# Optimization experiments

Hardware: AMD Instinct MI355X
Metric: run time of the kernel (lower is better)

The kernel has to match this reference:

```python
import jax, jax.numpy as jnp
import numpy as np

H = 12          # num_attention_heads
D = 64          # attention_head_size
HID = H * D     # hidden_size = 768
M = 1024        # max_position_embeddings


def setup_inputs() -> dict:
    key = jax.random.key(0)
    ks = jax.random.split(key, 9)
    B, S = 4, 1024
    s = 0.02
    return {
        "hidden_states": jax.random.normal(ks[0], (B, S, HID), jnp.float32),
        "attention_mask": jnp.zeros((B, 1, 1, S), jnp.float32),
        "Wq": jax.random.normal(ks[1], (HID, HID), jnp.float32) * s,
        "bq": jnp.zeros((HID,), jnp.float32),
        "Wk": jax.random.normal(ks[2], (HID, HID), jnp.float32) * s,
        "bk": jnp.zeros((HID,), jnp.float32),
        "Wv": jax.random.normal(ks[3], (HID, HID), jnp.float32) * s,
        "bv": jnp.zeros((HID,), jnp.float32),
        "dist_emb": jax.random.normal(ks[4], (2 * M - 1, D), jnp.float32) * s,
    }


def reference(hidden_states, attention_mask, Wq, bq, Wk, bk, Wv, bv, dist_emb):
    B, S, _ = hidden_states.shape

    def heads(x):  # [B,S,HID] -> [B,H,S,D]
        return x.reshape(B, S, H, D).transpose(0, 2, 1, 3)

    q = heads(hidden_states @ Wq + bq)
    k = heads(hidden_states @ Wk + bk)
    v = heads(hidden_states @ Wv + bv)

    # raw dot-product scores [B,H,S,S]
    scores = jnp.einsum('bhld,bhrd->bhlr', q, k)

    # relative_key_query positional bias
    pos = jnp.arange(S)
    distance = pos[:, None] - pos[None, :] + (M - 1)   # [S,S] in [0, 2M-2]
    pe = dist_emb[distance]                            # [S,S,D]
    scores = scores + jnp.einsum('bhld,lrd->bhlr', q, pe) \
                    + jnp.einsum('bhrd,lrd->bhlr', k, pe)

    scores = scores / jnp.sqrt(jnp.asarray(D, scores.dtype)) + attention_mask
    probs = jax.nn.softmax(scores, axis=-1)            # dropout is identity in eval

    ctx = jnp.einsum('bhlr,bhrd->bhld', probs, v)      # [B,H,S,D]
    ctx = ctx.transpose(0, 2, 1, 3).reshape(B, S, HID)
    return ctx, probs
```

## Files before the change

### kernel.cpp

```cpp
#include <hip/hip_runtime.h>
#include <hip/hip_bf16.h>

#define DEVFN __device__ __forceinline__

typedef __bf16 bf16x8 __attribute__((ext_vector_type(8)));
typedef float f32x4 __attribute__((ext_vector_type(4)));
typedef unsigned short ushort8 __attribute__((ext_vector_type(8)));
typedef unsigned short us4 __attribute__((ext_vector_type(4)));

namespace {

constexpr int S = 1024;
constexpr int HID = 768;
constexpr int NH = 12;
constexpr int HD = 64;
constexpr float SC = 0.4246609f;
constexpr float LOG2E = 1.44269504f;

DEVFN unsigned short f2bf(float f) {
  union { float f; unsigned u; } v; v.f = f;
  unsigned r = v.u + 0x7FFF + ((v.u >> 16) & 1);
  return (unsigned short)(r >> 16);
}

DEVFN float bf2f(unsigned short u) {
  union { unsigned u; float f; } v; v.u = ((unsigned)u) << 16; return v.f;
}

DEVFN f32x4 zero4() { return f32x4{0.f, 0.f, 0.f, 0.f}; }

DEVFN f32x4 mfma_bf16(bf16x8 a, bf16x8 b, f32x4 c) {
  return __builtin_amdgcn_mfma_f32_16x16x32_bf16(a, b, c, 0, 0, 0);
}

DEVFN void gload16(void* lds_base, const void* gsrc) {
  __builtin_amdgcn_global_load_lds(
      (const __attribute__((address_space(1))) void*)gsrc,
      (__attribute__((address_space(3))) void*)lds_base, 16, 0, 0);
}

DEVFN bf16x8 frag_ld(const char* tile, int row, int ch) {
  int chs = ch ^ (row & 7);
  return *(const bf16x8*)(tile + row * 128 + chs * 16);
}

__global__ void k0_cvt_x(const float* __restrict__ x, unsigned short* __restrict__ xb) {
  size_t i = (size_t)(blockIdx.x * 256 + threadIdx.x) * 8;
  float4 a = *(const float4*)(x + i);
  float4 c = *(const float4*)(x + i + 4);
  ushort8 o;
  o[0] = f2bf(a.x); o[1] = f2bf(a.y); o[2] = f2bf(a.z); o[3] = f2bf(a.w);
  o[4] = f2bf(c.x); o[5] = f2bf(c.y); o[6] = f2bf(c.z); o[7] = f2bf(c.w);
  *(ushort8*)(xb + i) = o;
}

__global__ void k0_cvt_pe(const float* __restrict__ de, unsigned short* __restrict__ peb) {
  size_t i = (size_t)(blockIdx.x * 256 + threadIdx.x) * 8;
  int row = (int)(i >> 6);
  ushort8 o;
  if (row < 2047) {
    float4 a = *(const float4*)(de + i);
    float4 c = *(const float4*)(de + i + 4);
    o[0] = f2bf(a.x * SC); o[1] = f2bf(a.y * SC); o[2] = f2bf(a.z * SC); o[3] = f2bf(a.w * SC);
    o[4] = f2bf(c.x * SC); o[5] = f2bf(c.y * SC); o[6] = f2bf(c.z * SC); o[7] = f2bf(c.w * SC);
  } else {
    o = ushort8{0, 0, 0, 0, 0, 0, 0, 0};
  }
  *(ushort8*)(peb + i) = o;
}

__global__ __launch_bounds__(256) void k0_wt(const float* __restrict__ Wq,
                                             const float* __restrict__ Wk,
                                             const float* __restrict__ Wv,
                                             unsigned short* __restrict__ wt) {
  __shared__ float t[64][65];
  int bidx = blockIdx.x;
  int sec = bidx / 144, rem = bidx % 144;
  int ktb = rem / 12, ntb = rem % 12;
  const float* W = (sec == 0) ? Wq : ((sec == 1) ? Wk : Wv);
  int k0 = ktb * 64, n0 = ntb * 64;
  int tid = threadIdx.x;
  #pragma unroll
  for (int p = 0; p < 4; ++p) {
    int id = p * 256 + tid;
    int row = id >> 4, ch = id & 15;
    float4 v = *(const float4*)(W + (size_t)(k0 + row) * 768 + n0 + ch * 4);
    t[row][ch * 4 + 0] = v.x; t[row][ch * 4 + 1] = v.y;
    t[row][ch * 4 + 2] = v.z; t[row][ch * 4 + 3] = v.w;
  }
  __syncthreads();
  #pragma unroll
  for (int p = 0; p < 2; ++p) {
    int id = p * 256 + tid;
    int nrow = id >> 3, c8 = id & 7;
    ushort8 o;
    #pragma unroll
    for (int i = 0; i < 8; ++i) o[i] = f2bf(t[c8 * 8 + i][nrow]);
    *(ushort8*)(wt + (size_t)(sec * 768 + n0 + nrow) * 768 + k0 + c8 * 8) = o;
  }
}

__global__ __launch_bounds__(256) void k1_qkv(
    const unsigned short* __restrict__ xb, const unsigned short* __restrict__ wt,
    const float* __restrict__ bq, const float* __restrict__ bk, const float* __restrict__ bv,
    unsigned short* __restrict__ q_ws, unsigned short* __restrict__ k_ws,
    unsigned short* __restrict__ vt_ws) {
  __shared__ char ldsA[8192], ldsB[8192];
  const int tid = threadIdx.x, lane = tid & 63, wv = tid >> 6;
  const int row16 = lane & 15, cgrp = lane >> 4;
  const int ntb = blockIdx.x % 36, mtb = blockIdx.x / 36;
  const int sec = ntb / 12;
  const int n0 = ntb * 64;
  const int m0 = mtb * 64;

  f32x4 acc[4] = {zero4(), zero4(), zero4(), zero4()};

  for (int k0 = 0; k0 < 768; k0 += 64) {
    #pragma unroll
    for (int c = 0; c < 2; ++c) {
      int cc = (wv * 2 + c) * 64 + lane;
      int row = cc >> 3, ch = cc & 7, chs = ch ^ (row & 7);
      gload16(ldsA + (wv * 2 + c) * 1024, xb + (size_t)(m0 + row) * 768 + k0 + chs * 8);
      gload16(ldsB + (wv * 2 + c) * 1024, wt + (size_t)(n0 + row) * 768 + k0 + chs * 8);
    }
    __syncthreads();
    if (sec < 2) {
      bf16x8 af[2];
      #pragma unroll
      for (int k2 = 0; k2 < 2; ++k2) af[k2] = frag_ld(ldsA, wv * 16 + row16, k2 * 4 + cgrp);
      #pragma unroll
      for (int nt = 0; nt < 4; ++nt)
        #pragma unroll
        for (int k2 = 0; k2 < 2; ++k2) {
          bf16x8 bf = frag_ld(ldsB, nt * 16 + row16, k2 * 4 + cgrp);
          acc[nt] = mfma_bf16(af[k2], bf, acc[nt]);
        }
    } else {
      bf16x8 af[2];
      #pragma unroll
      for (int k2 = 0; k2 < 2; ++k2) af[k2] = frag_ld(ldsB, wv * 16 + row16, k2 * 4 + cgrp);
      #pragma unroll
      for (int mt = 0; mt < 4; ++mt)
        #pragma unroll
        for (int k2 = 0; k2 < 2; ++k2) {
          bf16x8 bx = frag_ld(ldsA, mt * 16 + row16, k2 * 4 + cgrp);
          acc[mt] = mfma_bf16(af[k2], bx, acc[mt]);
        }
    }
    __syncthreads();
  }

  if (sec < 2) {
    unsigned short* dst = (sec == 0) ? q_ws : k_ws;
    const float* bias = (sec == 0) ? bq : bk;
    int nl0 = (ntb % 12) * 64;
    #pragma unroll
    for (int nt = 0; nt < 4; ++nt) {
      int nn = nl0 + nt * 16 + row16;
      float bb = bias[nn];
      int hh = nn >> 6, dd = nn & 63;
      #pragma unroll
      for (int j = 0; j < 4; ++j) {
        int m = m0 + wv * 16 + cgrp * 4 + j;
        int b_ = m >> 10, s_ = m & 1023;
        dst[(size_t)((b_ * 12 + hh) * 1024 + s_) * 64 + dd] = f2bf((acc[nt][j] + bb) * SC);
      }
    }
  } else {
    int nl0 = (ntb % 12) * 64;
    #pragma unroll
    for (int j = 0; j < 4; ++j) {
      int nn = nl0 + wv * 16 + cgrp * 4 + j;
      float bb = bv[nn];
      int hh = nn >> 6, dd = nn & 63;
      #pragma unroll
      for (int mt = 0; mt < 4; ++mt) {
        int m = m0 + mt * 16 + row16;
        int b_ = m >> 10, s_ = m & 1023;
        vt_ws[(size_t)((b_ * 12 + hh) * 64 + dd) * 1024 + s_] = f2bf(acc[mt][j] + bb);
      }
    }
  }
}

__global__ __launch_bounds__(512) void k2_score(
    const unsigned short* __restrict__ q_ws, const unsigned short* __restrict__ k_ws,
    const unsigned short* __restrict__ peb, const float* __restrict__ mask,
    unsigned short* __restrict__ p_out, float* __restrict__ rsum_part) {
  __shared__ __align__(16) char stage_lds[40960];
  __shared__ unsigned short p_sh[2][64 * 64];
  __shared__ float rsum_sh[4][64];

  const int tid = threadIdx.x, lane = tid & 63;
  const int wv8 = tid >> 6;
  const int quad = wv8 >> 2;
  const int wv = wv8 & 3;
  const int wl = wv >> 1, wr = wv & 1;
  const int row16 = lane & 15, cgrp = lane >> 4;

  const int bid = blockIdx.x;
  const int swz = (bid & 7) * 768 + (bid >> 3);
  const int rq = swz & 7, lt = (swz >> 3) & 15, bh = swz >> 7;
  const int b = bh / NH;
  const int l0 = lt * 64;
  const int rt = rq * 2 + quad;
  const int r0 = rt * 64;

  const unsigned short* qh = q_ws + (size_t)bh * S * HD;
  const unsigned short* khp = k_ws + (size_t)bh * S * HD;
  const float* maskb = mask + b * S;

  char* k_lds = stage_lds + quad * 8192;
  char* pe_lds = stage_lds + 16384;
  const int peoff = 64 * (1 - quad);

  #pragma unroll
  for (int c = 0; c < 2; ++c) {
    int cc = (wv * 2 + c) * 64 + lane;
    int row = cc >> 3, ch = cc & 7, chs = ch ^ (row & 7);
    gload16(k_lds + (wv * 2 + c) * 1024, khp + (size_t)(r0 + row) * HD + chs * 8);
  }
  {
    int mU = l0 - rq * 128 - 64 + 960;
    #pragma unroll
    for (int c = 0; c < 3; ++c) {
      int cc = (wv8 * 3 + c) * 64 + lane;
      int row = cc >> 3, ch = cc & 7, chs = ch ^ (row & 7);
      gload16(pe_lds + (wv8 * 3 + c) * 1024, peb + (size_t)(mU + row) * HD + chs * 8);
    }
  }

  bf16x8 qf[2][2];
  #pragma unroll
  for (int ltl = 0; ltl < 2; ++ltl)
    #pragma unroll
    for (int k2 = 0; k2 < 2; ++k2)
      qf[ltl][k2] = *(const bf16x8*)(qh + (size_t)(l0 + wl * 32 + ltl * 16 + row16) * HD +
                                     k2 * 32 + cgrp * 8);
  __syncthreads();

  bf16x8 kf[2][2], pef[4][2];
  #pragma unroll
  for (int rtl = 0; rtl < 2; ++rtl)
    #pragma unroll
    for (int k2 = 0; k2 < 2; ++k2)
      kf[rtl][k2] = frag_ld(k_lds, wr * 32 + rtl * 16 + row16, k2 * 4 + cgrp);
  const int qb = (wl - wr) * 32 + 32 + peoff;
  #pragma unroll
  for (int jt = 0; jt < 4; ++jt)
    #pragma unroll
    for (int k2 = 0; k2 < 2; ++k2)
      pef[jt][k2] = frag_ld(pe_lds, qb + jt * 16 + row16, k2 * 4 + cgrp);
  __syncthreads();

  unsigned short* s3w = (unsigned short*)stage_lds + wv8 * (64 * 36);

  #pragma unroll
  for (int rtl = 0; rtl < 2; ++rtl)
    #pragma unroll
    for (int jt = 0; jt < 4; ++jt) {
      f32x4 a3 = zero4();
      a3 = mfma_bf16(kf[rtl][0], pef[jt][0], a3);
      a3 = mfma_bf16(kf[rtl][1], pef[jt][1], a3);
      us4 o;
      o[0] = f2bf(a3[0]); o[1] = f2bf(a3[1]); o[2] = f2bf(a3[2]); o[3] = f2bf(a3[3]);
      *(us4*)(s3w + (jt * 16 + row16) * 36 + rtl * 16 + cgrp * 4) = o;
    }

  f32x4 s1[2][2];
  #pragma unroll
  for (int ltl = 0; ltl < 2; ++ltl)
    #pragma unroll
    for (int rtl = 0; rtl < 2; ++rtl) {
      f32x4 a1 = zero4();
      a1 = mfma_bf16(qf[ltl][0], kf[rtl][0], a1);
      a1 = mfma_bf16(qf[ltl][1], kf[rtl][1], a1);
      s1[ltl][rtl] = a1;
    }
  f32x4 s2[2][4];
  #pragma unroll
  for (int ltl = 0; ltl < 2; ++ltl)
    #pragma unroll
    for (int jt = 0; jt < 4; ++jt) {
      f32x4 a2 = zero4();
      a2 = mfma_bf16(qf[ltl][0], pef[jt][0], a2);
      a2 = mfma_bf16(qf[ltl][1], pef[jt][1], a2);
      s2[ltl][jt] = a2;
    }

  float rs[2][4] = {};
  #pragma unroll
  for (int rtl = 0; rtl < 2; ++rtl) {
    float mval = maskb[r0 + wr * 32 + rtl * 16 + row16] * LOG2E;
    #pragma unroll
    for (int ltl = 0; ltl < 2; ++ltl) {
      const int jtA = ltl - rtl + 1;
      #pragma unroll
      for (int j = 0; j < 4; ++j) {
        int dl = ltl * 16 + cgrp * 4 + j;
        int dr = rtl * 16 + row16;
        int jjq = dl - dr + 31;
        int src = (lane & 48) | (jjq & 15);
        float vA = __shfl(s2[ltl][jtA][j], src, 64);
        float vB = __shfl(s2[ltl][jtA + 1][j], src, 64);
        float b1 = ((jjq >> 4) == jtA) ? vA : vB;
        float b2 = bf2f(s3w[jjq * 36 + dr]);
        float p = exp2f(s1[ltl][rtl][j] + b1 + b2 + mval);
        rs[ltl][j] += p;
        int dlb = wl * 32 + dl, drb = wr * 32 + dr;
        p_sh[quad][dlb * 64 + (drb ^ ((dlb & 7) << 3))] = f2bf(p);
      }
    }
  }

  #pragma unroll
  for (int ltl = 0; ltl < 2; ++ltl)
    #pragma unroll
    for (int j = 0; j < 4; ++j) {
      float v = rs[ltl][j];
      v += __shfl_xor(v, 1, 64);
      v += __shfl_xor(v, 2, 64);
      v += __shfl_xor(v, 4, 64);
      v += __shfl_xor(v, 8, 64);
      rs[ltl][j] = v;
    }
  if (row16 == 0) {
    #pragma unroll
    for (int ltl = 0; ltl < 2; ++ltl)
      #pragma unroll
      for (int j = 0; j < 4; ++j)
        rsum_sh[quad * 2 + wr][wl * 32 + ltl * 16 + cgrp * 4 + j] = rs[ltl][j];
  }
  __syncthreads();

  if (tid < 64)
    rsum_part[((size_t)(bh * 16 + lt) * 64 + tid) * 8 + rq] =
        rsum_sh[0][tid] + rsum_sh[1][tid] + rsum_sh[2][tid] + rsum_sh[3][tid];

  {
    const int t256 = tid & 255;
    #pragma unroll
    for (int p2 = 0; p2 < 2; ++p2) {
      int id = p2 * 256 + t256, dl = id >> 3, c = id & 7;
      uint4 w = *(const uint4*)((const char*)p_sh[quad] + dl * 128 + (c ^ (dl & 7)) * 16);
      *(uint4*)(p_out + ((size_t)bh * S + l0 + dl) * S + r0 + c * 8) = w;
    }
  }
}

__global__ __launch_bounds__(256) void k3_pv(
    const unsigned short* __restrict__ p_in, const unsigned short* __restrict__ vt_ws,
    const float* __restrict__ rsum_part, float* __restrict__ out_ctx,
    float* __restrict__ out_probs) {
  __shared__ char p_sh[2][8192];
  __shared__ float inv_sh[64];

  const int tid = threadIdx.x, lane = tid & 63, wv = tid >> 6;
  const int row16 = lane & 15, cgrp = lane >> 4;
  const int bid = blockIdx.x;
  const int swz = (bid & 7) * 96 + (bid >> 3);
  const int lt = swz & 15, bh = swz >> 4;
  const int b = bh / NH, h = bh % NH;
  const int l0 = lt * 64;

  const unsigned short* vth = vt_ws + (size_t)bh * HD * S;
  float* probs_bh = out_probs + (size_t)bh * S * S;

  if (tid < 64) {
    const float4* pp =
        (const float4*)(rsum_part + ((size_t)(bh * 16 + lt) * 64 + tid) * 8);
    float4 v0 = pp[0], v1 = pp[1];
    inv_sh[tid] = 1.0f / (v0.x + v0.y + v0.z + v0.w + v1.x + v1.y + v1.z + v1.w);
  }

  auto stage = [&](char* buf, int r0) {
    #pragma unroll
    for (int c = 0; c < 2; ++c) {
      int cc = (wv * 2 + c) * 64 + lane;
      int row = cc >> 3, ch = cc & 7, chs = ch ^ (row & 7);
      gload16(buf + (wv * 2 + c) * 1024,
              p_in + ((size_t)bh * S + l0 + row) * S + r0 + chs * 8);
    }
  };

  stage(p_sh[0], 0);
  __syncthreads();

  f32x4 ctxacc[4] = {zero4(), zero4(), zero4(), zero4()};

  for (int rt = 0; rt < 16; ++rt) {
    const int r0 = rt * 64, cur = rt & 1;
    if (rt < 15) stage(p_sh[cur ^ 1], r0 + 64);
    const char* cb = p_sh[cur];

    #pragma unroll
    for (int p2 = 0; p2 < 2; ++p2) {
      int id = p2 * 256 + tid, dl = id >> 3, c = id & 7;
      uint4 w = *(const uint4*)(cb + dl * 128 + (c ^ (dl & 7)) * 16);
      const unsigned short* pu = (const unsigned short*)&w;
      float iv = inv_sh[dl];
      float* dst = probs_bh + (size_t)(l0 + dl) * S + r0 + c * 8;
      float4 lo{bf2f(pu[0]) * iv, bf2f(pu[1]) * iv, bf2f(pu[2]) * iv, bf2f(pu[3]) * iv};
      float4 hi{bf2f(pu[4]) * iv, bf2f(pu[5]) * iv, bf2f(pu[6]) * iv, bf2f(pu[7]) * iv};
      *(float4*)dst = lo; *(float4*)(dst + 4) = hi;
    }

    {
      int lrow = wv * 16 + row16;
      bf16x8 pa[2];
      #pragma unroll
      for (int kc = 0; kc < 2; ++kc) {
        int ch = kc * 4 + cgrp, chs = ch ^ (lrow & 7);
        pa[kc] = *(const bf16x8*)(cb + lrow * 128 + chs * 16);
      }
      #pragma unroll
      for (int dt = 0; dt < 4; ++dt) {
        bf16x8 vb0 = *(const bf16x8*)(vth + (size_t)(dt * 16 + row16) * S + r0 + cgrp * 8);
        bf16x8 vb1 = *(const bf16x8*)(vth + (size_t)(dt * 16 + row16) * S + r0 + 32 + cgrp * 8);
        ctxacc[dt] = mfma_bf16(pa[0], vb0, ctxacc[dt]);
        ctxacc[dt] = mfma_bf16(pa[1], vb1, ctxacc[dt]);
      }
    }
    __syncthreads();
  }

  #pragma unroll
  for (int dt = 0; dt < 4; ++dt)
    #pragma unroll
    for (int j = 0; j < 4; ++j) {
      int lr = wv * 16 + cgrp * 4 + j;
      out_ctx[((size_t)(b * S + l0 + lr)) * HID + h * HD + dt * 16 + row16] =
          ctxacc[dt][j] * inv_sh[lr];
    }
}

}

extern "C" void kernel_launch(void* const* d_in, const int* in_sizes, int n_in,
                              void* d_out, int out_size, void* d_ws, size_t ws_size,
                              hipStream_t stream) {
  const float* hidden = (const float*)d_in[0];
  const float* mask   = (const float*)d_in[1];
  const float* Wq = (const float*)d_in[2];
  const float* bq = (const float*)d_in[3];
  const float* Wk = (const float*)d_in[4];
  const float* bk = (const float*)d_in[5];
  const float* Wv = (const float*)d_in[6];
  const float* bv = (const float*)d_in[7];
  const float* de = (const float*)d_in[8];

  unsigned short* ws = (unsigned short*)d_ws;
  unsigned short* q_ws  = ws;
  unsigned short* k_ws  = ws + 3145728;
  unsigned short* vt_ws = ws + 6291456;
  unsigned short* xb    = ws + 9437184;
  unsigned short* wt    = ws + 12582912;
  unsigned short* peb   = ws + 14352384;
  float* rsum_part = (float*)(ws + 14483456);
  unsigned short* p_ws  = ws + 16056320;

  float* outc = (float*)d_out;
  float* outp = outc + (size_t)4 * 1024 * 768;

  hipLaunchKernelGGL(k0_cvt_x, dim3(1536), dim3(256), 0, stream, hidden, xb);
  hipLaunchKernelGGL(k0_cvt_pe, dim3(64), dim3(256), 0, stream, de, peb);
  hipLaunchKernelGGL(k0_wt, dim3(432), dim3(256), 0, stream, Wq, Wk, Wv, wt);
  hipLaunchKernelGGL(k1_qkv, dim3(2304), dim3(256), 0, stream,
                     xb, wt, bq, bk, bv, q_ws, k_ws, vt_ws);
  hipLaunchKernelGGL(k2_score, dim3(6144), dim3(512), 0, stream,
                     q_ws, k_ws, peb, mask, p_ws, rsum_part);
  hipLaunchKernelGGL(k3_pv, dim3(768), dim3(256), 0, stream,
                     p_ws, vt_ws, rsum_part, outc, outp);
}
```

Baseline: 200.3 us.

## Split probs normalization out of PV kernel into separate wide elementwise kernel

Moves the fp32 probs write (bf16 P times the inverse row sum) out of the PV kernel into its own elementwise kernel with 24576 blocks. A small kernel computes the inverse row sums once into a workspace buffer. Both the PV and normalization kernels read from that buffer. The PV kernel, which had only 768 blocks, no longer carries the large 200MB store stream, so the store can use the full GPU. The cost is two extra launches and a second read of the bf16 P matrix from memory.

```diff
diff --git a/kernel.cpp b/kernel.cpp
--- a/kernel.cpp
+++ b/kernel.cpp
@@ -348,10 +348,17 @@
   }
 }
 
-__global__ __launch_bounds__(256) void k3_pv(
+__global__ __launch_bounds__(256) void k_inv(const float* __restrict__ rsum_part,
+                                             float* __restrict__ inv_ws) {
+  int t = blockIdx.x * 256 + threadIdx.x;
+  const float4* pp = (const float4*)(rsum_part + (size_t)t * 8);
+  float4 v0 = pp[0], v1 = pp[1];
+  inv_ws[t] = 1.0f / (v0.x + v0.y + v0.z + v0.w + v1.x + v1.y + v1.z + v1.w);
+}
+
+__global__ __launch_bounds__(256) void k3p_pv(
     const unsigned short* __restrict__ p_in, const unsigned short* __restrict__ vt_ws,
-    const float* __restrict__ rsum_part, float* __restrict__ out_ctx,
-    float* __restrict__ out_probs) {
+    const float* __restrict__ inv_ws, float* __restrict__ out_ctx) {
   __shared__ char p_sh[2][8192];
   __shared__ float inv_sh[64];
 
@@ -364,14 +371,8 @@
   const int l0 = lt * 64;
 
   const unsigned short* vth = vt_ws + (size_t)bh * HD * S;
-  float* probs_bh = out_probs + (size_t)bh * S * S;
-
-  if (tid < 64) {
-    const float4* pp =
-        (const float4*)(rsum_part + ((size_t)(bh * 16 + lt) * 64 + tid) * 8);
-    float4 v0 = pp[0], v1 = pp[1];
-    inv_sh[tid] = 1.0f / (v0.x + v0.y + v0.z + v0.w + v1.x + v1.y + v1.z + v1.w);
-  }
+
+  if (tid < 64) inv_sh[tid] = inv_ws[(size_t)(bh * 16 + lt) * 64 + tid];
 
   auto stage = [&](char* buf, int r0) {
     #pragma unroll
@@ -393,33 +394,19 @@
     if (rt < 15) stage(p_sh[cur ^ 1], r0 + 64);
     const char* cb = p_sh[cur];
 
-    #pragma unroll
-    for (int p2 = 0; p2 < 2; ++p2) {
-      int id = p2 * 256 + tid, dl = id >> 3, c = id & 7;
-      uint4 w = *(const uint4*)(cb + dl * 128 + (c ^ (dl & 7)) * 16);
-      const unsigned short* pu = (const unsigned short*)&w;
-      float iv = inv_sh[dl];
-      float* dst = probs_bh + (size_t)(l0 + dl) * S + r0 + c * 8;
-      float4 lo{bf2f(pu[0]) * iv, bf2f(pu[1]) * iv, bf2f(pu[2]) * iv, bf2f(pu[3]) * iv};
-      float4 hi{bf2f(pu[4]) * iv, bf2f(pu[5]) * iv, bf2f(pu[6]) * iv, bf2f(pu[7]) * iv};
-      *(float4*)dst = lo; *(float4*)(dst + 4) = hi;
-    }
-
-    {
-      int lrow = wv * 16 + row16;
-      bf16x8 pa[2];
-      #pragma unroll
-      for (int kc = 0; kc < 2; ++kc) {
-        int ch = kc * 4 + cgrp, chs = ch ^ (lrow & 7);
-        pa[kc] = *(const bf16x8*)(cb + lrow * 128 + chs * 16);
-      }
-      #pragma unroll
-      for (int dt = 0; dt < 4; ++dt) {
-        bf16x8 vb0 = *(const bf16x8*)(vth + (size_t)(dt * 16 + row16) * S + r0 + cgrp * 8);
-        bf16x8 vb1 = *(const bf16x8*)(vth + (size_t)(dt * 16 + row16) * S + r0 + 32 + cgrp * 8);
-        ctxacc[dt] = mfma_bf16(pa[0], vb0, ctxacc[dt]);
-        ctxacc[dt] = mfma_bf16(pa[1], vb1, ctxacc[dt]);
-      }
+    int lrow = wv * 16 + row16;
+    bf16x8 pa[2];
+    #pragma unroll
+    for (int kc = 0; kc < 2; ++kc) {
+      int ch = kc * 4 + cgrp, chs = ch ^ (lrow & 7);
+      pa[kc] = *(const bf16x8*)(cb + lrow * 128 + chs * 16);
+    }
+    #pragma unroll
+    for (int dt = 0; dt < 4; ++dt) {
+      bf16x8 vb0 = *(const bf16x8*)(vth + (size_t)(dt * 16 + row16) * S + r0 + cgrp * 8);
+      bf16x8 vb1 = *(const bf16x8*)(vth + (size_t)(dt * 16 + row16) * S + r0 + 32 + cgrp * 8);
+      ctxacc[dt] = mfma_bf16(pa[0], vb0, ctxacc[dt]);
+      ctxacc[dt] = mfma_bf16(pa[1], vb1, ctxacc[dt]);
     }
     __syncthreads();
   }
@@ -432,6 +419,21 @@
       out_ctx[((size_t)(b * S + l0 + lr)) * HID + h * HD + dt * 16 + row16] =
           ctxacc[dt][j] * inv_sh[lr];
     }
+}
+
+__global__ __launch_bounds__(256) void k3n(const unsigned short* __restrict__ p_in,
+                                           const float* __restrict__ inv_ws,
+                                           float* __restrict__ out_probs) {
+  int gid = blockIdx.x * 256 + threadIdx.x;
+  int row = gid >> 7;
+  int c = gid & 127;
+  float iv = inv_ws[row];
+  ushort8 w = *(const ushort8*)(p_in + (size_t)row * 1024 + c * 8);
+  float* dst = out_probs + (size_t)row * 1024 + c * 8;
+  float4 lo{bf2f(w[0]) * iv, bf2f(w[1]) * iv, bf2f(w[2]) * iv, bf2f(w[3]) * iv};
+  float4 hi{bf2f(w[4]) * iv, bf2f(w[5]) * iv, bf2f(w[6]) * iv, bf2f(w[7]) * iv};
+  *(float4*)dst = lo;
+  *(float4*)(dst + 4) = hi;
 }
 
 }
@@ -458,6 +460,7 @@
   unsigned short* peb   = ws + 14352384;
   float* rsum_part = (float*)(ws + 14483456);
   unsigned short* p_ws  = ws + 16056320;
+  float* inv_ws = (float*)(ws + 66387968);
 
   float* outc = (float*)d_out;
   float* outp = outc + (size_t)4 * 1024 * 768;
@@ -469,6 +472,8 @@
                      xb, wt, bq, bk, bv, q_ws, k_ws, vt_ws);
   hipLaunchKernelGGL(k2_score, dim3(6144), dim3(512), 0, stream,
                      q_ws, k_ws, peb, mask, p_ws, rsum_part);
-  hipLaunchKernelGGL(k3_pv, dim3(768), dim3(256), 0, stream,
-                     p_ws, vt_ws, rsum_part, outc, outp);
-}
+  hipLaunchKernelGGL(k_inv, dim3(192), dim3(256), 0, stream, rsum_part, inv_ws);
+  hipLaunchKernelGGL(k3p_pv, dim3(768), dim3(256), 0, stream,
+                     p_ws, vt_ws, inv_ws, outc);
+  hipLaunchKernelGGL(k3n, dim3(24576), dim3(256), 0, stream, p_ws, inv_ws, outp);
+}
```

Measured after the change: 223.7 us. 1.12x slower.
